# Performance work log

Measured on AMD Instinct MI355X. Metric: run time of the kernel, lower is better.

The kernel has to match this reference:

```python
import jax, jax.numpy as jnp
import numpy as np

# Four fixed 3x3 'gradient' kernels (left, right, up, down), stacked as OIHW (4,1,3,3).
_K = np.zeros((4, 1, 3, 3), np.float32)
_K[0, 0, 1, 0] = -1.0; _K[0, 0, 1, 1] = 1.0   # left:  center - left neighbor
_K[1, 0, 1, 1] = 1.0;  _K[1, 0, 1, 2] = -1.0  # right: center - right neighbor
_K[2, 0, 0, 1] = -1.0; _K[2, 0, 1, 1] = 1.0   # up:    center - upper neighbor
_K[3, 0, 1, 1] = 1.0;  _K[3, 0, 2, 1] = -1.0  # down:  center - lower neighbor
KERNELS = jnp.asarray(_K)

LOSS_WEIGHT = 1.0
POOL = 4


def _avgpool4(x):
    # AvgPool2d(4) on NCHW with H,W divisible by 4
    b, c, h, w = x.shape
    return x.reshape(b, c, h // POOL, POOL, w // POOL, POOL).mean(axis=(3, 5))


def _grad_conv(x):
    # F.conv2d(x, kernels, padding=1); x: (B,1,Hp,Wp) -> (B,4,Hp,Wp)
    return jax.lax.conv_general_dilated(
        x, KERNELS, window_strides=(1, 1), padding=((1, 1), (1, 1)),
        dimension_numbers=('NCHW', 'OIHW', 'NCHW'))


def setup_inputs() -> dict:
    key = jax.random.key(0)
    k1, k2 = jax.random.split(key)
    B, C, H, W = 32, 3, 512, 512
    x = jax.random.uniform(k1, (B, C, H, W), dtype=jnp.float32)
    pred = jax.random.uniform(k2, (B, C, H, W), dtype=jnp.float32)
    return {"x": x, "pred": pred}


def reference(x, pred):
    # channel mean -> (B,1,H,W), then 4x4 average pool -> (B,1,H/4,W/4)
    org_pool = _avgpool4(jnp.mean(x, axis=1, keepdims=True))
    enh_pool = _avgpool4(jnp.mean(pred, axis=1, keepdims=True))
    # NOTE: the original computes weight_diff and E_1 but never uses them in the
    # returned loss, so they are omitted (no effect on output or gradients).
    d = _grad_conv(org_pool) - _grad_conv(enh_pool)  # (B,4,Hp,Wp)
    # mean(D_left + D_right + D_up + D_down) == mean over (B,Hp,Wp) of channel-sum
    E = jnp.mean(jnp.sum(d * d, axis=1))
    return LOSS_WEIGHT * E
```

## Files before the change

### kernel.cpp

```cpp
#include <hip/hip_runtime.h>

constexpr int B  = 32;
constexpr int C  = 3;
constexpr int H  = 512;
constexpr int W  = 512;
constexpr int HP = H / 4;
constexpr int WP = W / 4;
constexpr int NP = B * HP * WP;
constexpr int W4 = W / 4;

constexpr int ROWS_PB    = 8;
constexpr int BLK_PER_IMG = HP / ROWS_PB;
constexpr int NBLOCKS    = B * BLK_PER_IMG;

__global__ __launch_bounds__(256, 2) void spatial_loss_fused(
        const float* __restrict__ x,
        const float* __restrict__ pred,
        float* __restrict__ out) {
    __shared__ float pt[ROWS_PB + 1][WP];

    int orig = blockIdx.x;
    int blk  = (orig & 7) * (NBLOCKS / 8) + (orig >> 3);
    int b    = blk >> 4;
    int br   = blk & 15;
    int tid  = threadIdx.x;
    int q    = tid & 127;
    int h    = tid >> 7;

    const float4* __restrict__ xb = (const float4*)x;
    const float4* __restrict__ pb = (const float4*)pred;

    int row0 = br * 32 + h * 16;
    #pragma unroll
    for (int j = 0; j < 4; ++j) {
        int base = (b * C * H + row0 + 4 * j) * W4 + q;
        float s0 = 0.0f, s1 = 0.0f;
        #pragma unroll
        for (int c = 0; c < C; ++c) {
            int a = base + c * H * W4;
            float4 x0 = xb[a];
            float4 x1 = xb[a + W4];
            float4 x2 = xb[a + 2 * W4];
            float4 x3 = xb[a + 3 * W4];
            float4 p0 = pb[a];
            float4 p1 = pb[a + W4];
            float4 p2 = pb[a + 2 * W4];
            float4 p3 = pb[a + 3 * W4];
            s0 += (x0.x - p0.x) + (x0.y - p0.y) + (x0.z - p0.z) + (x0.w - p0.w);
            s1 += (x1.x - p1.x) + (x1.y - p1.y) + (x1.z - p1.z) + (x1.w - p1.w);
            s0 += (x2.x - p2.x) + (x2.y - p2.y) + (x2.z - p2.z) + (x2.w - p2.w);
            s1 += (x3.x - p3.x) + (x3.y - p3.y) + (x3.z - p3.z) + (x3.w - p3.w);
        }
        pt[1 + 4 * h + j][q] = (s0 + s1) * (1.0f / 48.0f);
    }

    if (tid < 128) {
        float s = 0.0f;
        if (br > 0) {
            int hr   = br * 32 - 4;
            int base = (b * C * H + hr) * W4 + tid;
            float s0 = 0.0f, s1 = 0.0f;
            #pragma unroll
            for (int c = 0; c < C; ++c) {
                int a = base + c * H * W4;
                float4 x0 = xb[a];
                float4 x1 = xb[a + W4];
                float4 x2 = xb[a + 2 * W4];
                float4 x3 = xb[a + 3 * W4];
                float4 p0 = pb[a];
                float4 p1 = pb[a + W4];
                float4 p2 = pb[a + 2 * W4];
                float4 p3 = pb[a + 3 * W4];
                s0 += (x0.x - p0.x) + (x0.y - p0.y) + (x0.z - p0.z) + (x0.w - p0.w);
                s1 += (x1.x - p1.x) + (x1.y - p1.y) + (x1.z - p1.z) + (x1.w - p1.w);
                s0 += (x2.x - p2.x) + (x2.y - p2.y) + (x2.z - p2.z) + (x2.w - p2.w);
                s1 += (x3.x - p3.x) + (x3.y - p3.y) + (x3.z - p3.z) + (x3.w - p3.w);
            }
            s = (s0 + s1) * (1.0f / 48.0f);
        }
        pt[0][tid] = s;
    }
    __syncthreads();

    float acc = 0.0f;
    #pragma unroll
    for (int j = 0; j < 4; ++j) {
        int row = 4 * h + j;
        int gy  = br * 8 + row;
        float c  = pt[row + 1][q];
        float up = pt[row][q];
        float lf = (q > 0) ? pt[row + 1][q - 1] : 0.0f;
        float dy = c - up;
        float dx = c - lf;
        float wy = (gy > 0) ? 2.0f : 1.0f;
        float wx = (q  > 0) ? 2.0f : 1.0f;
        acc += wy * dy * dy + wx * dx * dx;
        if (gy == HP - 1) acc += c * c;
        if (q  == WP - 1) acc += c * c;
    }

    #pragma unroll
    for (int off = 32; off > 0; off >>= 1)
        acc += __shfl_down(acc, off, 64);

    __shared__ float ws_red[4];
    int lane = tid & 63;
    int wid  = tid >> 6;
    if (lane == 0) ws_red[wid] = acc;
    __syncthreads();
    if (tid == 0) {
        float s = ws_red[0] + ws_red[1] + ws_red[2] + ws_red[3];
        atomicAdd(out, s * (1.0f / (float)NP));
    }
}

extern "C" void kernel_launch(void* const* d_in, const int* in_sizes, int n_in,
                              void* d_out, int out_size, void* d_ws, size_t ws_size,
                              hipStream_t stream) {
    const float* x    = (const float*)d_in[0];
    const float* pred = (const float*)d_in[1];
    float* out = (float*)d_out;

    hipMemsetAsync(out, 0, sizeof(float), stream);

    spatial_loss_fused<<<NBLOCKS, 256, 0, stream>>>(x, pred, out);
}
```

Measured before the change: 219.9 us.

## Spread per-channel pooled-row tasks across 1024 threads per block

Each block now runs 1024 threads and splits the pooling work into independent (channel, pooled row, column) tasks, so every thread issues only eight float4 loads instead of twenty-four. Per-channel partial sums go to shared memory and are combined in a second pass before the gradient stage, which gives one pooled pixel per thread. The aim is more memory-level parallelism and more loads in flight for this bandwidth-bound kernel. The cost is an extra shared-memory pass, an extra barrier and larger blocks, which may limit occupancy.

```diff
diff --git a/kernel.cpp b/kernel.cpp
--- a/kernel.cpp
+++ b/kernel.cpp
@@ -9,35 +9,39 @@
 constexpr int NP = B * HP * WP;
 constexpr int W4 = W / 4;
 
-constexpr int ROWS_PB    = 8;
+constexpr int ROWS_PB     = 8;
+constexpr int HROWS       = ROWS_PB + 1;
 constexpr int BLK_PER_IMG = HP / ROWS_PB;
-constexpr int NBLOCKS    = B * BLK_PER_IMG;
+constexpr int NBLOCKS     = B * BLK_PER_IMG;
+constexpr int NTASK       = C * HROWS * WP;
 
-__global__ __launch_bounds__(256, 2) void spatial_loss_fused(
+__global__ __launch_bounds__(1024, 8) void spatial_loss_fused(
         const float* __restrict__ x,
         const float* __restrict__ pred,
         float* __restrict__ out) {
-    __shared__ float pt[ROWS_PB + 1][WP];
+    __shared__ float sm[C * HROWS][WP];
+    __shared__ float P[HROWS][WP];
+    __shared__ float ws_red[16];
 
     int orig = blockIdx.x;
     int blk  = (orig & 7) * (NBLOCKS / 8) + (orig >> 3);
     int b    = blk >> 4;
     int br   = blk & 15;
+    int py0  = br * ROWS_PB;
     int tid  = threadIdx.x;
-    int q    = tid & 127;
-    int h    = tid >> 7;
 
     const float4* __restrict__ xb = (const float4*)x;
     const float4* __restrict__ pb = (const float4*)pred;
 
-    int row0 = br * 32 + h * 16;
-    #pragma unroll
-    for (int j = 0; j < 4; ++j) {
-        int base = (b * C * H + row0 + 4 * j) * W4 + q;
-        float s0 = 0.0f, s1 = 0.0f;
-        #pragma unroll
-        for (int c = 0; c < C; ++c) {
-            int a = base + c * H * W4;
+    for (int t = tid; t < NTASK; t += 1024) {
+        int q  = t & 127;
+        int cr = t >> 7;
+        int rr = cr / 3;
+        int c  = cr - 3 * rr;
+        int gy = py0 + rr - 1;
+        float s = 0.0f;
+        if (gy >= 0) {
+            int a = ((b * C + c) * H + gy * 4) * W4 + q;
             float4 x0 = xb[a];
             float4 x1 = xb[a + W4];
             float4 x2 = xb[a + 2 * W4];
@@ -46,70 +50,53 @@
             float4 p1 = pb[a + W4];
             float4 p2 = pb[a + 2 * W4];
             float4 p3 = pb[a + 3 * W4];
-            s0 += (x0.x - p0.x) + (x0.y - p0.y) + (x0.z - p0.z) + (x0.w - p0.w);
-            s1 += (x1.x - p1.x) + (x1.y - p1.y) + (x1.z - p1.z) + (x1.w - p1.w);
-            s0 += (x2.x - p2.x) + (x2.y - p2.y) + (x2.z - p2.z) + (x2.w - p2.w);
-            s1 += (x3.x - p3.x) + (x3.y - p3.y) + (x3.z - p3.z) + (x3.w - p3.w);
+            float s0 = (x0.x - p0.x) + (x0.y - p0.y) + (x0.z - p0.z) + (x0.w - p0.w);
+            float s1 = (x1.x - p1.x) + (x1.y - p1.y) + (x1.z - p1.z) + (x1.w - p1.w);
+            float s2 = (x2.x - p2.x) + (x2.y - p2.y) + (x2.z - p2.z) + (x2.w - p2.w);
+            float s3 = (x3.x - p3.x) + (x3.y - p3.y) + (x3.z - p3.z) + (x3.w - p3.w);
+            s = (s0 + s1) + (s2 + s3);
         }
-        pt[1 + 4 * h + j][q] = (s0 + s1) * (1.0f / 48.0f);
-    }
-
-    if (tid < 128) {
-        float s = 0.0f;
-        if (br > 0) {
-            int hr   = br * 32 - 4;
-            int base = (b * C * H + hr) * W4 + tid;
-            float s0 = 0.0f, s1 = 0.0f;
-            #pragma unroll
-            for (int c = 0; c < C; ++c) {
-                int a = base + c * H * W4;
-                float4 x0 = xb[a];
-                float4 x1 = xb[a + W4];
-                float4 x2 = xb[a + 2 * W4];
-                float4 x3 = xb[a + 3 * W4];
-                float4 p0 = pb[a];
-                float4 p1 = pb[a + W4];
-                float4 p2 = pb[a + 2 * W4];
-                float4 p3 = pb[a + 3 * W4];
-                s0 += (x0.x - p0.x) + (x0.y - p0.y) + (x0.z - p0.z) + (x0.w - p0.w);
-                s1 += (x1.x - p1.x) + (x1.y - p1.y) + (x1.z - p1.z) + (x1.w - p1.w);
-                s0 += (x2.x - p2.x) + (x2.y - p2.y) + (x2.z - p2.z) + (x2.w - p2.w);
-                s1 += (x3.x - p3.x) + (x3.y - p3.y) + (x3.z - p3.z) + (x3.w - p3.w);
-            }
-            s = (s0 + s1) * (1.0f / 48.0f);
-        }
-        pt[0][tid] = s;
+        sm[cr][q] = s;
     }
     __syncthreads();
 
-    float acc = 0.0f;
-    #pragma unroll
-    for (int j = 0; j < 4; ++j) {
-        int row = 4 * h + j;
-        int gy  = br * 8 + row;
-        float c  = pt[row + 1][q];
-        float up = pt[row][q];
-        float lf = (q > 0) ? pt[row + 1][q - 1] : 0.0f;
-        float dy = c - up;
-        float dx = c - lf;
+    for (int i = tid; i < HROWS * WP; i += 1024) {
+        int q  = i & 127;
+        int pr = i >> 7;
+        P[pr][q] = (sm[3 * pr][q] + sm[3 * pr + 1][q] + sm[3 * pr + 2][q])
+                   * (1.0f / 48.0f);
+    }
+    __syncthreads();
+
+    float acc;
+    {
+        int q  = tid & 127;
+        int r  = tid >> 7;
+        int gy = py0 + r;
+        float cv = P[r + 1][q];
+        float up = P[r][q];
+        float lf = (q > 0) ? P[r + 1][q - 1] : 0.0f;
+        float dy = cv - up;
+        float dx = cv - lf;
         float wy = (gy > 0) ? 2.0f : 1.0f;
         float wx = (q  > 0) ? 2.0f : 1.0f;
-        acc += wy * dy * dy + wx * dx * dx;
-        if (gy == HP - 1) acc += c * c;
-        if (q  == WP - 1) acc += c * c;
+        acc = wy * dy * dy + wx * dx * dx;
+        if (gy == HP - 1) acc += cv * cv;
+        if (q  == WP - 1) acc += cv * cv;
     }
 
     #pragma unroll
     for (int off = 32; off > 0; off >>= 1)
         acc += __shfl_down(acc, off, 64);
 
-    __shared__ float ws_red[4];
     int lane = tid & 63;
     int wid  = tid >> 6;
     if (lane == 0) ws_red[wid] = acc;
     __syncthreads();
     if (tid == 0) {
-        float s = ws_red[0] + ws_red[1] + ws_red[2] + ws_red[3];
+        float s = 0.0f;
+        #pragma unroll
+        for (int k = 0; k < 16; ++k) s += ws_red[k];
         atomicAdd(out, s * (1.0f / (float)NP));
     }
 }
@@ -123,5 +110,5 @@
 
     hipMemsetAsync(out, 0, sizeof(float), stream);
 
-    spatial_loss_fused<<<NBLOCKS, 256, 0, stream>>>(x, pred, out);
+    spatial_loss_fused<<<NBLOCKS, 1024, 0, stream>>>(x, pred, out);
 }
```

After: 221.7 us. No clear change (+0.8%).
